# Performance work log

Measured on AMD Instinct MI355X. Metric: run time of the kernel, lower is better.

Reference implementation:

```python
import jax, jax.numpy as jnp
import numpy as np

PAD = 0
SOS = 1
NEG = -1e9


def _lstm_scan(x, Wih, Whh, b, h0, c0, reverse=False):
    # x: [T, B, in]; torch gate order i, f, g, o
    def step(carry, xt):
        h, c = carry
        g = xt @ Wih.T + h @ Whh.T + b
        i, f, gg, o = jnp.split(g, 4, axis=-1)
        c = jax.nn.sigmoid(f) * c + jax.nn.sigmoid(i) * jnp.tanh(gg)
        h = jax.nn.sigmoid(o) * jnp.tanh(c)
        return (h, c), h
    (hT, cT), hs = jax.lax.scan(step, (h0, c0), x, reverse=reverse)
    return hs, hT, cT


def setup_inputs() -> dict:
    B, Ts, Tt = 32, 64, 66
    E, H, V = 512, 512, 16000
    key = jax.random.key(0)
    ks = jax.random.split(key, 16)
    s = 0.05
    n = lambda k, shape: (jax.random.normal(k, shape, dtype=jnp.float32) * s)
    return {
        'src_sentences': jax.random.randint(ks[0], (B, Ts), 4, V),
        'trg_sentences': jax.random.randint(ks[1], (B, Tt), 4, V),
        'src_emb': n(ks[2], (V, E)),
        'trg_emb': n(ks[3], (V, E)),
        'enc0_Wih': n(ks[4], (2, 4 * H, E)),
        'enc0_Whh': n(ks[5], (2, 4 * H, H)),
        'enc0_b': n(ks[6], (2, 4 * H)),
        'enc1_Wih': n(ks[7], (2, 4 * H, 2 * H)),
        'enc1_Whh': n(ks[8], (2, 4 * H, H)),
        'enc1_b': n(ks[9], (2, 4 * H)),
        'dec_Wih': n(ks[10], (8 * H, E)),      # LSTMCell: hidden = 2H -> 4*(2H) gates
        'dec_Whh': n(ks[11], (8 * H, 2 * H)),
        'dec_b': n(ks[12], (8 * H)),
        'out_W1': n(ks[13], (H, 4 * H)),
        'out_W2': n(ks[14], (V - 4, H)),
    }


def reference(src_sentences, trg_sentences, src_emb, trg_emb,
              enc0_Wih, enc0_Whh, enc0_b, enc1_Wih, enc1_Whh, enc1_b,
              dec_Wih, dec_Whh, dec_b, out_W1, out_W2):
    B, Ts = src_sentences.shape
    Tt = trg_sentences.shape[1]
    H = out_W1.shape[0]
    dt = src_emb.dtype
    enc_mask = src_sentences == PAD            # [B, Ts] (all False here)

    # ---- encoder: 2-layer bidirectional LSTM (dropout inactive / eval) ----
    x = jnp.swapaxes(src_emb[src_sentences], 0, 1)   # [Ts, B, E]
    z = jnp.zeros((B, H), dt)
    hf0, hfT, cfT = _lstm_scan(x, enc0_Wih[0], enc0_Whh[0], enc0_b[0], z, z)
    hb0, hbT, cbT = _lstm_scan(x, enc0_Wih[1], enc0_Whh[1], enc0_b[1], z, z, reverse=True)
    x1 = jnp.concatenate([hf0, hb0], axis=-1)        # [Ts, B, 2H]
    hf1, _, _ = _lstm_scan(x1, enc1_Wih[0], enc1_Whh[0], enc1_b[0], z, z)
    hb1, _, _ = _lstm_scan(x1, enc1_Wih[1], enc1_Whh[1], enc1_b[1], z, z, reverse=True)
    enc_out = jnp.swapaxes(jnp.concatenate([hf1, hb1], axis=-1), 0, 1)  # [B, Ts, 2H]
    # module uses encoder_hidden_t[0], [1] -> layer-0 fwd/bwd final states
    hidden = jnp.concatenate([hfT, hbT], axis=-1)    # [B, 2H]
    cell = jnp.concatenate([cfT, cbT], axis=-1)

    # ---- decoder: teacher_force = 1.0 (deterministic) ----
    steps = Tt - 2
    emb_in = jnp.swapaxes(trg_emb[trg_sentences[:, :steps]], 0, 1)  # [steps, B, E]
    tgts = jnp.swapaxes(trg_sentences[:, 1:steps + 1], 0, 1)        # [steps, B]

    def step(carry, inp):
        h, c, loss = carry
        xt, tgt = inp
        g = xt @ dec_Wih.T + h @ dec_Whh.T + dec_b
        i, f, gg, o = jnp.split(g, 4, axis=-1)
        c = jax.nn.sigmoid(f) * c + jax.nn.sigmoid(i) * jnp.tanh(gg)
        h = jax.nn.sigmoid(o) * jnp.tanh(c)
        dmask = tgt == PAD
        h = jnp.where(dmask[:, None], jnp.zeros((), dt), h)  # decoder_hidden_t[mask] = 0
        # dot attention over encoder states
        scores = jnp.einsum('btd,bd->bt', enc_out, h)
        scores = jnp.where(enc_mask, NEG, scores)
        attn = jax.nn.softmax(scores, axis=1)
        ctx = jnp.einsum('bt,btd->bd', attn, enc_out)
        zt = jnp.tanh(jnp.concatenate([h, ctx], axis=-1) @ out_W1.T)
        logits = zt @ out_W2.T                                # [B, V-4]
        logp = jax.nn.log_softmax(logits, axis=1)
        tgt_idx = tgt - 4
        valid = tgt_idx != -4                                 # ignore_index=-4 (PAD)
        safe = jnp.where(valid, tgt_idx, 0)
        nll = -jnp.take_along_axis(logp, safe[:, None], axis=1)[:, 0]
        loss = loss + jnp.sum(jnp.where(valid, nll, jnp.zeros((), dt)))
        pred = jnp.argmax(logits, axis=1) + 4
        return (h, c, loss), pred

    (_, _, loss), preds = jax.lax.scan(step, (hidden, cell, jnp.zeros((), dt)), (emb_in, tgts))
    denom = jnp.sum(trg_sentences[:, 1:-1] != PAD).astype(dt)
    return loss / denom, preds.T  # preds: [B, steps]
```

## Files before the change

kernel.cpp:

```cpp
#include <hip/hip_runtime.h>
#include <hip/hip_bf16.h>
#include <math.h>

#define TSRC 64
#define TTRG 66
#define NVOC 15996
#define NTILE 125

__device__ __forceinline__ float sigm(float x){ return 1.f/(1.f+expf(-x)); }

struct GArgs {
  const float* A;  int lda;
  const float* Bw; int ldb;
  const float* bias;
  float* C; int ldc;
  int N; int K; int nNb; int act;
};

template<int BM,int BN,int BK,int TM,int TN>
__global__ __launch_bounds__(256)
void k_gemm(GArgs a)
{
  const int tid = threadIdx.x;
  const int mb = blockIdx.x / a.nNb;
  const int nb = blockIdx.x % a.nNb;
  const int m0 = mb*BM, n0 = nb*BN;
  const float* A  = a.A + (size_t)m0*a.lda;
  const float* Bw = a.Bw;

  __shared__ float As[BK][BM+1];
  __shared__ float Bs[BK][BN+4];
  const int tx = tid % (BN/TN);
  const int ty = tid / (BN/TN);
  float acc[TM][TN];
  #pragma unroll
  for (int i=0;i<TM;i++)
    #pragma unroll
    for (int j=0;j<TN;j++) acc[i][j]=0.f;

  for (int kt=0; kt<a.K; kt+=BK) {
    #pragma unroll
    for (int i=tid; i<BM*BK; i+=256) {
      int m = i/BK, k = i%BK;
      As[k][m] = A[(size_t)m*a.lda + kt + k];
    }
    #pragma unroll
    for (int i=tid; i<BN*BK; i+=256) {
      int n = i/BK, k = i%BK;
      int gn = n0+n;
      Bs[k][n] = (gn < a.N) ? Bw[(size_t)gn*a.ldb + kt + k] : 0.f;
    }
    __syncthreads();
    #pragma unroll
    for (int k=0;k<BK;k++) {
      float av[TM], bv[TN];
      #pragma unroll
      for (int i=0;i<TM;i++) av[i]=As[k][ty*TM+i];
      #pragma unroll
      for (int j=0;j<TN;j++) bv[j]=Bs[k][tx*TN+j];
      #pragma unroll
      for (int i=0;i<TM;i++)
        #pragma unroll
        for (int j=0;j<TN;j++)
          acc[i][j] = fmaf(av[i], bv[j], acc[i][j]);
    }
    __syncthreads();
  }
  #pragma unroll
  for (int i=0;i<TM;i++) {
    int m = m0 + ty*TM + i;
    #pragma unroll
    for (int j=0;j<TN;j++) {
      int n = n0 + tx*TN + j;
      if (n < a.N) {
        float v = acc[i][j];
        if (a.bias) v += a.bias[n];
        if (a.act)  v = tanhf(v);
        a.C[(size_t)m*a.ldc + n] = v;
      }
    }
  }
}

__global__ __launch_bounds__(256)
void k_logits(const float* __restrict__ A, const float* __restrict__ Bw,
              const int* __restrict__ trg,
              float* __restrict__ Pmax, int* __restrict__ Parg,
              float* __restrict__ Psum, float* __restrict__ Ltgt)
{
  const int tid = threadIdx.x;
  const int mb = blockIdx.x / NTILE;
  const int nb = blockIdx.x % NTILE;
  const int m0 = mb*128, n0 = nb*128;

  __shared__ float As[16][129];
  __shared__ float Bs[16][132];
  const int tx = tid & 15;
  const int ty = tid >> 4;
  float acc[8][8];
  #pragma unroll
  for (int i=0;i<8;i++)
    #pragma unroll
    for (int j=0;j<8;j++) acc[i][j]=0.f;

  for (int kt=0; kt<512; kt+=16) {
    #pragma unroll
    for (int i=tid; i<128*16; i+=256) {
      int m = i>>4, k = i&15;
      As[k][m] = A[(size_t)(m0+m)*512 + kt + k];
    }
    #pragma unroll
    for (int i=tid; i<128*16; i+=256) {
      int n = i>>4, k = i&15;
      int gn = n0+n;
      Bs[k][n] = (gn < NVOC) ? Bw[(size_t)gn*512 + kt + k] : 0.f;
    }
    __syncthreads();
    #pragma unroll
    for (int k=0;k<16;k++) {
      float av[8], bv[8];
      #pragma unroll
      for (int i=0;i<8;i++) av[i]=As[k][ty*8+i];
      #pragma unroll
      for (int j=0;j<8;j++) bv[j]=Bs[k][tx*8+j];
      #pragma unroll
      for (int i=0;i<8;i++)
        #pragma unroll
        for (int j=0;j<8;j++)
          acc[i][j] = fmaf(av[i], bv[j], acc[i][j]);
    }
    __syncthreads();
  }

  #pragma unroll
  for (int i=0;i<8;i++) {
    int r = m0 + ty*8 + i;
    int step = r >> 5, b = r & 31;
    int tgt = trg[b*TTRG + step + 1];
    int ti = tgt - 4;
    float m = -3.4e38f; int am = 0x7fffffff;
    #pragma unroll
    for (int j=0;j<8;j++) {
      int gn = n0 + tx*8 + j;
      if (gn < NVOC) {
        float x = acc[i][j];
        if (x > m || (x == m && gn < am)) { m = x; am = gn; }
      }
    }
    float s = 0.f;
    float lt = 0.f;
    #pragma unroll
    for (int j=0;j<8;j++) {
      int gn = n0 + tx*8 + j;
      if (gn < NVOC) {
        s += expf(acc[i][j] - m);
        if (gn == ti) lt = acc[i][j];
      }
    }
    #pragma unroll
    for (int d=1; d<16; d<<=1) {
      float m2 = __shfl_xor(m, d);
      int   a2 = __shfl_xor(am, d);
      float s2 = __shfl_xor(s, d);
      float l2 = __shfl_xor(lt, d);
      float M = fmaxf(m, m2);
      s = s*expf(m - M) + s2*expf(m2 - M);
      if (m2 > m || (m2 == m && a2 < am)) am = a2;
      m = M;
      lt += l2;
    }
    if (tx == 0) {
      size_t pi = (size_t)r*NTILE + nb;
      Pmax[pi] = m; Parg[pi] = am; Psum[pi] = s;
      if (ti >= n0 && ti < n0 + 128) Ltgt[r] = lt;
    }
  }
}

__global__ __launch_bounds__(128)
void k_combine(const float* __restrict__ Pmax, const int* __restrict__ Parg,
               const float* __restrict__ Psum, const float* __restrict__ Ltgt,
               const int* __restrict__ trg,
               float* __restrict__ nll, float* __restrict__ outp)
{
  int r = blockIdx.x;
  int step = r >> 5, b = r & 31;
  int tid = threadIdx.x;
  __shared__ float sm[128]; __shared__ int sa[128]; __shared__ float ssum[128];
  float m = -3.4e38f; int am = 0x7fffffff; float s = 0.f;
  if (tid < NTILE) {
    size_t pi = (size_t)r*NTILE + tid;
    m = Pmax[pi]; am = Parg[pi]; s = Psum[pi];
  }
  sm[tid]=m; sa[tid]=am; ssum[tid]=s; __syncthreads();
  for (int off=64; off; off>>=1) {
    if (tid < off) {
      float m2 = sm[tid+off]; int a2 = sa[tid+off]; float s2 = ssum[tid+off];
      float m1 = sm[tid];     int a1 = sa[tid];     float s1 = ssum[tid];
      float M = fmaxf(m1, m2);
      ssum[tid] = s1*expf(m1 - M) + s2*expf(m2 - M);
      if (m2 > m1 || (m2 == m1 && a2 < a1)) sa[tid] = a2;
      sm[tid] = M;
    }
    __syncthreads();
  }
  if (tid == 0) {
    int tgt = trg[b*TTRG + step + 1];
    float nl = 0.f;
    if (tgt != 0) nl = -(Ltgt[r] - sm[0] - logf(ssum[0]));
    nll[step*32 + b] = nl;
    outp[1 + b*64 + step] = (float)(sa[0] + 4);
  }
}

__global__ void k_gather(const float* __restrict__ emb, const int* __restrict__ tok,
                         float* __restrict__ outp, int Tfull)
{
  int r = blockIdx.x;
  int t = r >> 5, b = r & 31;
  int token = tok[b*Tfull + t];
  const float4* s = (const float4*)(emb + (size_t)token*512);
  float4* d = (float4*)(outp + (size_t)r*512);
  d[threadIdx.x] = s[threadIdx.x];
}

__global__ __launch_bounds__(256)
void k_rgemm_enc(const float* __restrict__ Whh,
                 const float* __restrict__ hin,
                 float* __restrict__ P)
{
  const int ks  = blockIdx.x >> 5;
  const int rem = blockIdx.x & 31;
  const int dir = rem >> 4;
  const int jt  = rem & 15;
  const int j0  = jt*32;
  const int tid = threadIdx.x;
  const int jcol = tid & 31;
  const int bq   = tid >> 5;
  __shared__ float ws[128][65];
  __shared__ float hs[64][36];
  const float* W = Whh + (size_t)dir*2048*512;
  const float* H = hin + (size_t)dir*32*512;
  float acc[4][4];
  #pragma unroll
  for (int g=0;g<4;g++)
    #pragma unroll
    for (int i=0;i<4;i++) acc[g][i]=0.f;

  for (int kt=ks*128; kt<ks*128+128; kt+=64) {
    for (int idx=tid; idx<128*64; idx+=256) {
      int r = idx >> 6, k = idx & 63;
      int gate = r >> 5, jc = r & 31;
      ws[r][k] = W[(size_t)(gate*512 + j0 + jc)*512 + kt + k];
    }
    for (int idx=tid; idx<32*64; idx+=256) {
      int b = idx >> 6, k = idx & 63;
      hs[k][b] = H[(size_t)b*512 + kt + k];
    }
    __syncthreads();
    #pragma unroll 8
    for (int k=0;k<64;k++) {
      float4 hv = *reinterpret_cast<const float4*>(&hs[k][bq*4]);
      #pragma unroll
      for (int g=0;g<4;g++) {
        float wv = ws[g*32+jcol][k];
        acc[g][0] = fmaf(hv.x, wv, acc[g][0]);
        acc[g][1] = fmaf(hv.y, wv, acc[g][1]);
        acc[g][2] = fmaf(hv.z, wv, acc[g][2]);
        acc[g][3] = fmaf(hv.w, wv, acc[g][3]);
      }
    }
    __syncthreads();
  }
  #pragma unroll
  for (int g=0;g<4;g++)
    #pragma unroll
    for (int i=0;i<4;i++)
      P[((size_t)(ks*2+dir)*32 + bq*4+i)*2048 + g*512 + j0 + jcol] = acc[g][i];
}

__global__ __launch_bounds__(256)
void k_enc_combine(const float* __restrict__ P, const float* __restrict__ xg,
                   float* __restrict__ cst, float* __restrict__ hout,
                   float* __restrict__ xout, int tf, int tb, int mode)
{
  int t = blockIdx.x*256 + threadIdx.x;
  int jh = t & 511, b = (t>>9)&31, dir = t>>14;
  int tt = dir ? tb : tf;
  const float* x = xg + ((size_t)tt*32 + b)*4096 + dir*2048;
  float g4[4];
  #pragma unroll
  for (int g=0; g<4; g++) {
    float s = 0.f;
    #pragma unroll
    for (int ks=0; ks<4; ks++)
      s += P[((size_t)(ks*2+dir)*32 + b)*2048 + g*512 + jh];
    g4[g] = s + x[g*512 + jh];
  }
  size_t ci = ((size_t)dir*32 + b)*512 + jh;
  float cn = sigm(g4[1])*cst[ci] + sigm(g4[0])*tanhf(g4[2]);
  float hn = sigm(g4[3])*tanhf(cn);
  cst[ci] = cn;
  hout[ci] = hn;
  if (mode == 0) xout[((size_t)tt*32 + b)*1024 + dir*512 + jh] = hn;
  else           xout[((size_t)b*64 + tt)*1024 + dir*512 + jh] = hn;
}

__global__ void k_pack(const float* __restrict__ hfin, const float* __restrict__ cfin,
                       float* __restrict__ dh, float* __restrict__ dcc)
{
  int tid = blockIdx.x*256 + threadIdx.x;
  int j = tid & 1023, b = tid >> 10;
  int dir = j >> 9, jj = j & 511;
  size_t si = ((size_t)dir*32 + b)*512 + jj;
  dh[(size_t)b*1024 + j]  = hfin[si];
  dcc[(size_t)b*1024 + j] = cfin[si];
}

__global__ __launch_bounds__(256)
void k_rgemm_dec(const float* __restrict__ Whh,
                 const float* __restrict__ hin,
                 float* __restrict__ P)
{
  const int ks = blockIdx.x >> 5;
  const int jt = blockIdx.x & 31;
  const int j0 = jt*32;
  const int tid = threadIdx.x;
  const int jcol = tid & 31;
  const int bq   = tid >> 5;
  __shared__ float ws[128][65];
  __shared__ float hs[64][36];
  float acc[4][4];
  #pragma unroll
  for (int g=0;g<4;g++)
    #pragma unroll
    for (int i=0;i<4;i++) acc[g][i]=0.f;

  for (int kt=ks*128; kt<ks*128+128; kt+=64) {
    for (int idx=tid; idx<128*64; idx+=256) {
      int r = idx >> 6, k = idx & 63;
      int gate = r >> 5, jc = r & 31;
      ws[r][k] = Whh[(size_t)(gate*1024 + j0 + jc)*1024 + kt + k];
    }
    for (int idx=tid; idx<32*64; idx+=256) {
      int b = idx >> 6, k = idx & 63;
      hs[k][b] = hin[(size_t)b*1024 + kt + k];
    }
    __syncthreads();
    #pragma unroll 8
    for (int k=0;k<64;k++) {
      float4 hv = *reinterpret_cast<const float4*>(&hs[k][bq*4]);
      #pragma unroll
      for (int g=0;g<4;g++) {
        float wv = ws[g*32+jcol][k];
        acc[g][0] = fmaf(hv.x, wv, acc[g][0]);
        acc[g][1] = fmaf(hv.y, wv, acc[g][1]);
        acc[g][2] = fmaf(hv.z, wv, acc[g][2]);
        acc[g][3] = fmaf(hv.w, wv, acc[g][3]);
      }
    }
    __syncthreads();
  }
  #pragma unroll
  for (int g=0;g<4;g++)
    #pragma unroll
    for (int i=0;i<4;i++)
      P[((size_t)ks*32 + bq*4+i)*4096 + g*1024 + j0 + jcol] = acc[g][i];
}

__global__ __launch_bounds__(256)
void k_dec_combine(const float* __restrict__ P, const float* __restrict__ xg_t,
                   float* __restrict__ cst, float* __restrict__ hall_t,
                   const int* __restrict__ trg, int step)
{
  int t = blockIdx.x*256 + threadIdx.x;
  int jh = t & 1023, b = t >> 10;
  int tgt = trg[b*TTRG + step + 1];
  bool dm = (tgt == 0);
  const float* x = xg_t + (size_t)b*4096;
  float g4[4];
  #pragma unroll
  for (int g=0; g<4; g++) {
    float s = 0.f;
    #pragma unroll
    for (int ks=0; ks<8; ks++)
      s += P[((size_t)ks*32 + b)*4096 + g*1024 + jh];
    g4[g] = s + x[g*1024 + jh];
  }
  size_t ci = (size_t)b*1024 + jh;
  float cn = sigm(g4[1])*cst[ci] + sigm(g4[0])*tanhf(g4[2]);
  float hn = sigm(g4[3])*tanhf(cn);
  cst[ci] = cn;
  hall_t[ci] = dm ? 0.f : hn;
}

__global__ __launch_bounds__(256)
void k_attn(const float* __restrict__ Hall,
            const float* __restrict__ encout,
            const int* __restrict__ src,
            float* __restrict__ hctx)
{
  int bid = blockIdx.x;
  int t = bid >> 5, b = bid & 31;
  int tid = threadIdx.x;
  __shared__ float sh[1024];
  __shared__ float ssc[64];
  const float* h = Hall + ((size_t)t*32 + b)*1024;
  size_t row = (size_t)t*32 + b;
  #pragma unroll
  for (int r=0;r<4;r++) {
    int jh = tid + 256*r;
    float v = h[jh];
    sh[jh] = v;
    hctx[row*2048 + jh] = v;
  }
  __syncthreads();
  {
    int tq = tid >> 2, part = tid & 3;
    const float* eo = encout + ((size_t)b*64 + tq)*1024 + part*256;
    const float* hh = sh + part*256;
    float s = 0.f;
    for (int k=0;k<256;k++) s = fmaf(hh[k], eo[k], s);
    s += __shfl_xor(s, 1);
    s += __shfl_xor(s, 2);
    if (part == 0) ssc[tq] = (src[b*TSRC + tq] == 0) ? -1e9f : s;
  }
  __syncthreads();
  if (tid < 64) {
    float v = ssc[tid];
    float m = v;
    for (int d=1; d<64; d<<=1) m = fmaxf(m, __shfl_xor(m, d));
    float e = expf(v - m);
    float su = e;
    for (int d=1; d<64; d<<=1) su += __shfl_xor(su, d);
    ssc[tid] = e / su;
  }
  __syncthreads();
  #pragma unroll
  for (int r=0;r<4;r++) {
    int k = tid + 256*r;
    float a = 0.f;
    const float* eb = encout + (size_t)b*65536 + k;
    for (int tt=0;tt<64;tt++) a = fmaf(ssc[tt], eb[tt*1024], a);
    hctx[row*2048 + 1024 + k] = a;
  }
}

__global__ __launch_bounds__(256)
void k_final(const float* __restrict__ nll, const int* __restrict__ trg,
             float* __restrict__ outp)
{
  int tid = threadIdx.x;
  __shared__ float ss[256]; __shared__ int sc[256];
  float s = 0.f; int cnt = 0;
  for (int i=tid; i<2048; i+=256) {
    s += nll[i];
    int b = i >> 6, t = (i & 63) + 1;
    cnt += (trg[b*TTRG + t] != 0);
  }
  ss[tid]=s; sc[tid]=cnt; __syncthreads();
  for (int off=128; off; off>>=1) {
    if (tid<off) { ss[tid]+=ss[tid+off]; sc[tid]+=sc[tid+off]; }
    __syncthreads();
  }
  if (tid==0) outp[0] = ss[0] / (float)sc[0];
}

static void launch_big(hipStream_t st, const float* A, int lda,
                       const float* Bw, int ldb, const float* bias,
                       float* C, int ldc, int M, int N, int K, int act)
{
  GArgs a;
  a.A=A; a.lda=lda;
  a.Bw=Bw; a.ldb=ldb;
  a.bias=bias;
  a.C=C; a.ldc=ldc;
  a.N=N; a.K=K; a.nNb=(N+127)/128; a.act=act;
  dim3 g((M/128)*a.nNb, 1, 1);
  k_gemm<128,128,16,8,8><<<g, dim3(256), 0, st>>>(a);
}

static void launch_med(hipStream_t st, const float* A, int lda,
                       const float* Bw, int ldb, const float* bias,
                       float* C, int ldc, int M, int N, int K, int act)
{
  GArgs a;
  a.A=A; a.lda=lda;
  a.Bw=Bw; a.ldb=ldb;
  a.bias=bias;
  a.C=C; a.ldc=ldc;
  a.N=N; a.K=K; a.nNb=(N+63)/64; a.act=act;
  dim3 g((M/64)*a.nNb, 1, 1);
  k_gemm<64,64,16,4,4><<<g, dim3(256), 0, st>>>(a);
}

extern "C" void kernel_launch(void* const* d_in, const int* in_sizes, int n_in,
                              void* d_out, int out_size, void* d_ws, size_t ws_size,
                              hipStream_t stream)
{
  (void)in_sizes; (void)n_in; (void)out_size; (void)ws_size;
  const int*   src   = (const int*)  d_in[0];
  const int*   trg   = (const int*)  d_in[1];
  const float* semb  = (const float*)d_in[2];
  const float* temb  = (const float*)d_in[3];
  const float* e0Wih = (const float*)d_in[4];
  const float* e0Whh = (const float*)d_in[5];
  const float* e0b   = (const float*)d_in[6];
  const float* e1Wih = (const float*)d_in[7];
  const float* e1Whh = (const float*)d_in[8];
  const float* e1b   = (const float*)d_in[9];
  const float* dWih  = (const float*)d_in[10];
  const float* dWhh  = (const float*)d_in[11];
  const float* db    = (const float*)d_in[12];
  const float* W1    = (const float*)d_in[13];
  const float* W2    = (const float*)d_in[14];
  float* out = (float*)d_out;

  float* ws = (float*)d_ws;
  size_t o = 0;
  float* x_in   = ws + o; o += (size_t)2048*512;
  float* xg     = ws + o; o += (size_t)2048*4096;
  float* x1     = ws + o; o += (size_t)2048*1024;
  float* encout = ws + o; o += (size_t)2048*1024;
  float* hA     = ws + o; o += 2*32*512;
  float* hB     = ws + o; o += 2*32*512;
  float* cbuf   = ws + o; o += 2*32*512;
  float* dh0    = ws + o; o += 32*1024;
  float* dc     = ws + o; o += 32*1024;
  float* nll    = ws + o; o += 2048;
  float* P      = ws + o; o += (size_t)8*32*4096;
  float* Hall   = x1;
  float* hctx   = xg;
  float* zt     = x_in;
  float* Pmax   = xg + (size_t)4*1024*1024;
  int*   Parg   = (int*)(Pmax + (size_t)2048*NTILE);
  float* Psum   = Pmax + (size_t)2*2048*NTILE;
  float* Ltgt   = Pmax + (size_t)3*2048*NTILE;

  hipMemsetAsync(hA,   0, 2*32*512*sizeof(float), stream);
  hipMemsetAsync(cbuf, 0, 2*32*512*sizeof(float), stream);
  k_gather<<<dim3(2048), dim3(128), 0, stream>>>(semb, src, x_in, TSRC);
  launch_big(stream, x_in, 512, e0Wih, 512, e0b, xg, 4096, 2048, 4096, 512, 0);
  for (int s=0; s<64; s++) {
    float* hin  = (s&1) ? hB : hA;
    float* hout = (s&1) ? hA : hB;
    k_rgemm_enc<<<dim3(128), dim3(256), 0, stream>>>(e0Whh, hin, P);
    k_enc_combine<<<dim3(128), dim3(256), 0, stream>>>(P, xg, cbuf, hout, x1, s, 63-s, 0);
  }
  k_pack<<<dim3(128), dim3(256), 0, stream>>>(hA, cbuf, dh0, dc);

  hipMemsetAsync(hA,   0, 2*32*512*sizeof(float), stream);
  hipMemsetAsync(cbuf, 0, 2*32*512*sizeof(float), stream);
  launch_big(stream, x1, 1024, e1Wih, 1024, e1b, xg, 4096, 2048, 4096, 1024, 0);
  for (int s=0; s<64; s++) {
    float* hin  = (s&1) ? hB : hA;
    float* hout = (s&1) ? hA : hB;
    k_rgemm_enc<<<dim3(128), dim3(256), 0, stream>>>(e1Whh, hin, P);
    k_enc_combine<<<dim3(128), dim3(256), 0, stream>>>(P, xg, cbuf, hout, encout, s, 63-s, 1);
  }

  k_gather<<<dim3(2048), dim3(128), 0, stream>>>(temb, trg, x_in, TTRG);
  launch_big(stream, x_in, 512, dWih, 512, db, xg, 4096, 2048, 4096, 512, 0);
  for (int st=0; st<64; st++) {
    const float* hin = (st == 0) ? dh0 : (Hall + (size_t)(st-1)*32*1024);
    k_rgemm_dec<<<dim3(256), dim3(256), 0, stream>>>(dWhh, hin, P);
    k_dec_combine<<<dim3(128), dim3(256), 0, stream>>>(P, xg + (size_t)st*32*4096,
                 dc, Hall + (size_t)st*32*1024, trg, st);
  }

  k_attn<<<dim3(2048), dim3(256), 0, stream>>>(Hall, encout, src, hctx);
  launch_med(stream, hctx, 2048, W1, 2048, nullptr, zt, 512, 2048, 512, 2048, 1);
  k_logits<<<dim3(16*NTILE), dim3(256), 0, stream>>>(zt, W2, trg, Pmax, Parg, Psum, Ltgt);
  k_combine<<<dim3(2048), dim3(128), 0, stream>>>(Pmax, Parg, Psum, Ltgt, trg, nll, out);
  k_final<<<dim3(1), dim3(256), 0, stream>>>(nll, trg, out);
}
```

Before: 4.647 ms.

## Fuse recurrent LSTM steps into persistent kernels with grid barriers

Replaces the per-timestep launch pairs (recurrent GEMM plus gate combine) for both encoder layers and the decoder with single persistent kernels that loop over all 64 steps and use an atomic-counter grid barrier between phases. This removes about 384 kernel launches and their launch gaps. In exchange it relies on all 128/256 blocks being co-resident for the spin barrier to avoid deadlock. The weights are still reloaded from global memory every step, and each step now pays two barrier round trips.

```diff
diff --git a/kernel.cpp b/kernel.cpp
--- a/kernel.cpp
+++ b/kernel.cpp
@@ -8,6 +8,20 @@
 #define NTILE 125
 
 __device__ __forceinline__ float sigm(float x){ return 1.f/(1.f+expf(-x)); }
+
+__device__ __forceinline__ void grid_barrier(unsigned* cnt, unsigned nblk, unsigned& mygen)
+{
+  __syncthreads();
+  if (threadIdx.x == 0) {
+    __threadfence();
+    atomicAdd(cnt, 1u);
+    unsigned target = nblk * (mygen + 1u);
+    while (atomicAdd(cnt, 0u) < target) __builtin_amdgcn_s_sleep(2);
+    __threadfence();
+  }
+  __syncthreads();
+  mygen += 1u;
+}
 
 struct GArgs {
   const float* A;  int lda;
@@ -225,12 +239,17 @@
 }
 
 __global__ __launch_bounds__(256)
-void k_rgemm_enc(const float* __restrict__ Whh,
-                 const float* __restrict__ hin,
-                 float* __restrict__ P)
-{
-  const int ks  = blockIdx.x >> 5;
-  const int rem = blockIdx.x & 31;
+void k_enc_layer(const float* __restrict__ Whh,
+                 const float* __restrict__ xg,
+                 float* __restrict__ hA, float* __restrict__ hB,
+                 float* __restrict__ cst,
+                 float* __restrict__ P,
+                 float* __restrict__ xout, int mode,
+                 unsigned* __restrict__ cnt)
+{
+  const int bid = blockIdx.x;
+  const int ks  = bid >> 5;
+  const int rem = bid & 31;
   const int dir = rem >> 4;
   const int jt  = rem & 15;
   const int j0  = jt*32;
@@ -240,70 +259,77 @@
   __shared__ float ws[128][65];
   __shared__ float hs[64][36];
   const float* W = Whh + (size_t)dir*2048*512;
-  const float* H = hin + (size_t)dir*32*512;
-  float acc[4][4];
-  #pragma unroll
-  for (int g=0;g<4;g++)
-    #pragma unroll
-    for (int i=0;i<4;i++) acc[g][i]=0.f;
-
-  for (int kt=ks*128; kt<ks*128+128; kt+=64) {
-    for (int idx=tid; idx<128*64; idx+=256) {
-      int r = idx >> 6, k = idx & 63;
-      int gate = r >> 5, jc = r & 31;
-      ws[r][k] = W[(size_t)(gate*512 + j0 + jc)*512 + kt + k];
-    }
-    for (int idx=tid; idx<32*64; idx+=256) {
-      int b = idx >> 6, k = idx & 63;
-      hs[k][b] = H[(size_t)b*512 + kt + k];
-    }
-    __syncthreads();
-    #pragma unroll 8
-    for (int k=0;k<64;k++) {
-      float4 hv = *reinterpret_cast<const float4*>(&hs[k][bq*4]);
-      #pragma unroll
-      for (int g=0;g<4;g++) {
-        float wv = ws[g*32+jcol][k];
-        acc[g][0] = fmaf(hv.x, wv, acc[g][0]);
-        acc[g][1] = fmaf(hv.y, wv, acc[g][1]);
-        acc[g][2] = fmaf(hv.z, wv, acc[g][2]);
-        acc[g][3] = fmaf(hv.w, wv, acc[g][3]);
-      }
-    }
-    __syncthreads();
-  }
-  #pragma unroll
-  for (int g=0;g<4;g++)
-    #pragma unroll
-    for (int i=0;i<4;i++)
-      P[((size_t)(ks*2+dir)*32 + bq*4+i)*2048 + g*512 + j0 + jcol] = acc[g][i];
-}
-
-__global__ __launch_bounds__(256)
-void k_enc_combine(const float* __restrict__ P, const float* __restrict__ xg,
-                   float* __restrict__ cst, float* __restrict__ hout,
-                   float* __restrict__ xout, int tf, int tb, int mode)
-{
-  int t = blockIdx.x*256 + threadIdx.x;
-  int jh = t & 511, b = (t>>9)&31, dir = t>>14;
-  int tt = dir ? tb : tf;
-  const float* x = xg + ((size_t)tt*32 + b)*4096 + dir*2048;
-  float g4[4];
-  #pragma unroll
-  for (int g=0; g<4; g++) {
-    float s = 0.f;
-    #pragma unroll
-    for (int ks=0; ks<4; ks++)
-      s += P[((size_t)(ks*2+dir)*32 + b)*2048 + g*512 + jh];
-    g4[g] = s + x[g*512 + jh];
-  }
-  size_t ci = ((size_t)dir*32 + b)*512 + jh;
-  float cn = sigm(g4[1])*cst[ci] + sigm(g4[0])*tanhf(g4[2]);
-  float hn = sigm(g4[3])*tanhf(cn);
-  cst[ci] = cn;
-  hout[ci] = hn;
-  if (mode == 0) xout[((size_t)tt*32 + b)*1024 + dir*512 + jh] = hn;
-  else           xout[((size_t)b*64 + tt)*1024 + dir*512 + jh] = hn;
+  unsigned mygen = 0;
+
+  for (int s = 0; s < 64; ++s) {
+    const float* hin = (s&1) ? hB : hA;
+    float* hout      = (s&1) ? hA : hB;
+    const float* H = hin + (size_t)dir*32*512;
+    float acc[4][4];
+    #pragma unroll
+    for (int g=0;g<4;g++)
+      #pragma unroll
+      for (int i=0;i<4;i++) acc[g][i]=0.f;
+
+    for (int kh=0; kh<2; ++kh) {
+      int kt = ks*128 + kh*64;
+      for (int idx=tid; idx<128*64; idx+=256) {
+        int r = idx >> 6, k = idx & 63;
+        int gate = r >> 5, jc = r & 31;
+        ws[r][k] = W[(size_t)(gate*512 + j0 + jc)*512 + kt + k];
+      }
+      for (int idx=tid; idx<32*64; idx+=256) {
+        int b = idx >> 6, k = idx & 63;
+        hs[k][b] = H[(size_t)b*512 + kt + k];
+      }
+      __syncthreads();
+      #pragma unroll 8
+      for (int k=0;k<64;k++) {
+        float4 hv = *reinterpret_cast<const float4*>(&hs[k][bq*4]);
+        #pragma unroll
+        for (int g=0;g<4;g++) {
+          float wv = ws[g*32+jcol][k];
+          acc[g][0] = fmaf(hv.x, wv, acc[g][0]);
+          acc[g][1] = fmaf(hv.y, wv, acc[g][1]);
+          acc[g][2] = fmaf(hv.z, wv, acc[g][2]);
+          acc[g][3] = fmaf(hv.w, wv, acc[g][3]);
+        }
+      }
+      __syncthreads();
+    }
+    #pragma unroll
+    for (int g=0;g<4;g++)
+      #pragma unroll
+      for (int i=0;i<4;i++)
+        P[((size_t)(ks*2+dir)*32 + bq*4+i)*2048 + g*512 + j0 + jcol] = acc[g][i];
+
+    grid_barrier(cnt, 128u, mygen);
+
+    {
+      int t = bid*256 + tid;
+      int jh = t & 511, b = (t>>9)&31, d2 = t>>14;
+      int tt = d2 ? (63 - s) : s;
+      const float* x = xg + ((size_t)tt*32 + b)*4096 + d2*2048;
+      float g4[4];
+      #pragma unroll
+      for (int g=0; g<4; g++) {
+        float sum = 0.f;
+        #pragma unroll
+        for (int kk=0; kk<4; kk++)
+          sum += P[((size_t)(kk*2+d2)*32 + b)*2048 + g*512 + jh];
+        g4[g] = sum + x[g*512 + jh];
+      }
+      size_t ci = ((size_t)d2*32 + b)*512 + jh;
+      float cn = sigm(g4[1])*cst[ci] + sigm(g4[0])*tanhf(g4[2]);
+      float hn = sigm(g4[3])*tanhf(cn);
+      cst[ci] = cn;
+      hout[ci] = hn;
+      if (mode == 0) xout[((size_t)tt*32 + b)*1024 + d2*512 + jh] = hn;
+      else           xout[((size_t)b*64 + tt)*1024 + d2*512 + jh] = hn;
+    }
+
+    grid_barrier(cnt, 128u, mygen);
+  }
 }
 
 __global__ void k_pack(const float* __restrict__ hfin, const float* __restrict__ cfin,
@@ -318,9 +344,14 @@
 }
 
 __global__ __launch_bounds__(256)
-void k_rgemm_dec(const float* __restrict__ Whh,
-                 const float* __restrict__ hin,
-                 float* __restrict__ P)
+void k_dec_layer(const float* __restrict__ Whh,
+                 const float* __restrict__ xg,
+                 const float* __restrict__ dh0,
+                 float* __restrict__ cst,
+                 float* __restrict__ Hall,
+                 const int* __restrict__ trg,
+                 float* __restrict__ P,
+                 unsigned* __restrict__ cnt)
 {
   const int ks = blockIdx.x >> 5;
   const int jt = blockIdx.x & 31;
@@ -330,68 +361,74 @@
   const int bq   = tid >> 5;
   __shared__ float ws[128][65];
   __shared__ float hs[64][36];
-  float acc[4][4];
-  #pragma unroll
-  for (int g=0;g<4;g++)
-    #pragma unroll
-    for (int i=0;i<4;i++) acc[g][i]=0.f;
-
-  for (int kt=ks*128; kt<ks*128+128; kt+=64) {
-    for (int idx=tid; idx<128*64; idx+=256) {
-      int r = idx >> 6, k = idx & 63;
-      int gate = r >> 5, jc = r & 31;
-      ws[r][k] = Whh[(size_t)(gate*1024 + j0 + jc)*1024 + kt + k];
-    }
-    for (int idx=tid; idx<32*64; idx+=256) {
-      int b = idx >> 6, k = idx & 63;
-      hs[k][b] = hin[(size_t)b*1024 + kt + k];
-    }
-    __syncthreads();
-    #pragma unroll 8
-    for (int k=0;k<64;k++) {
-      float4 hv = *reinterpret_cast<const float4*>(&hs[k][bq*4]);
-      #pragma unroll
-      for (int g=0;g<4;g++) {
-        float wv = ws[g*32+jcol][k];
-        acc[g][0] = fmaf(hv.x, wv, acc[g][0]);
-        acc[g][1] = fmaf(hv.y, wv, acc[g][1]);
-        acc[g][2] = fmaf(hv.z, wv, acc[g][2]);
-        acc[g][3] = fmaf(hv.w, wv, acc[g][3]);
-      }
-    }
-    __syncthreads();
-  }
-  #pragma unroll
-  for (int g=0;g<4;g++)
-    #pragma unroll
-    for (int i=0;i<4;i++)
-      P[((size_t)ks*32 + bq*4+i)*4096 + g*1024 + j0 + jcol] = acc[g][i];
-}
-
-__global__ __launch_bounds__(256)
-void k_dec_combine(const float* __restrict__ P, const float* __restrict__ xg_t,
-                   float* __restrict__ cst, float* __restrict__ hall_t,
-                   const int* __restrict__ trg, int step)
-{
-  int t = blockIdx.x*256 + threadIdx.x;
-  int jh = t & 1023, b = t >> 10;
-  int tgt = trg[b*TTRG + step + 1];
-  bool dm = (tgt == 0);
-  const float* x = xg_t + (size_t)b*4096;
-  float g4[4];
-  #pragma unroll
-  for (int g=0; g<4; g++) {
-    float s = 0.f;
-    #pragma unroll
-    for (int ks=0; ks<8; ks++)
-      s += P[((size_t)ks*32 + b)*4096 + g*1024 + jh];
-    g4[g] = s + x[g*1024 + jh];
-  }
-  size_t ci = (size_t)b*1024 + jh;
-  float cn = sigm(g4[1])*cst[ci] + sigm(g4[0])*tanhf(g4[2]);
-  float hn = sigm(g4[3])*tanhf(cn);
-  cst[ci] = cn;
-  hall_t[ci] = dm ? 0.f : hn;
+  unsigned mygen = 0;
+
+  for (int st = 0; st < 64; ++st) {
+    const float* hin = (st == 0) ? dh0 : (Hall + (size_t)(st-1)*32*1024);
+    float acc[4][4];
+    #pragma unroll
+    for (int g=0;g<4;g++)
+      #pragma unroll
+      for (int i=0;i<4;i++) acc[g][i]=0.f;
+
+    for (int kh=0; kh<2; ++kh) {
+      int kt = ks*128 + kh*64;
+      for (int idx=tid; idx<128*64; idx+=256) {
+        int r = idx >> 6, k = idx & 63;
+        int gate = r >> 5, jc = r & 31;
+        ws[r][k] = Whh[(size_t)(gate*1024 + j0 + jc)*1024 + kt + k];
+      }
+      for (int idx=tid; idx<32*64; idx+=256) {
+        int b = idx >> 6, k = idx & 63;
+        hs[k][b] = hin[(size_t)b*1024 + kt + k];
+      }
+      __syncthreads();
+      #pragma unroll 8
+      for (int k=0;k<64;k++) {
+        float4 hv = *reinterpret_cast<const float4*>(&hs[k][bq*4]);
+        #pragma unroll
+        for (int g=0;g<4;g++) {
+          float wv = ws[g*32+jcol][k];
+          acc[g][0] = fmaf(hv.x, wv, acc[g][0]);
+          acc[g][1] = fmaf(hv.y, wv, acc[g][1]);
+          acc[g][2] = fmaf(hv.z, wv, acc[g][2]);
+          acc[g][3] = fmaf(hv.w, wv, acc[g][3]);
+        }
+      }
+      __syncthreads();
+    }
+    #pragma unroll
+    for (int g=0;g<4;g++)
+      #pragma unroll
+      for (int i=0;i<4;i++)
+        P[((size_t)ks*32 + bq*4+i)*4096 + g*1024 + j0 + jcol] = acc[g][i];
+
+    grid_barrier(cnt, 256u, mygen);
+
+    if (tid < 128) {
+      int t = blockIdx.x*128 + tid;
+      int jh = t & 1023, b = t >> 10;
+      int tgt = trg[b*TTRG + st + 1];
+      bool dm = (tgt == 0);
+      const float* x = xg + (size_t)st*32*4096 + (size_t)b*4096;
+      float g4[4];
+      #pragma unroll
+      for (int g=0; g<4; g++) {
+        float sum = 0.f;
+        #pragma unroll
+        for (int kk=0; kk<8; kk++)
+          sum += P[((size_t)kk*32 + b)*4096 + g*1024 + jh];
+        g4[g] = sum + x[g*1024 + jh];
+      }
+      size_t ci = (size_t)b*1024 + jh;
+      float cn = sigm(g4[1])*cst[ci] + sigm(g4[0])*tanhf(g4[2]);
+      float hn = sigm(g4[3])*tanhf(cn);
+      cst[ci] = cn;
+      Hall[(size_t)st*32*1024 + ci] = dm ? 0.f : hn;
+    }
+
+    grid_barrier(cnt, 256u, mygen);
+  }
 }
 
 __global__ __launch_bounds__(256)
@@ -529,6 +566,7 @@
   float* dc     = ws + o; o += 32*1024;
   float* nll    = ws + o; o += 2048;
   float* P      = ws + o; o += (size_t)8*32*4096;
+  unsigned* cnt = (unsigned*)(ws + o); o += 64;
   float* Hall   = x1;
   float* hctx   = xg;
   float* zt     = x_in;
@@ -537,36 +575,26 @@
   float* Psum   = Pmax + (size_t)2*2048*NTILE;
   float* Ltgt   = Pmax + (size_t)3*2048*NTILE;
 
+  hipMemsetAsync(cnt, 0, 64*sizeof(float), stream);
+
   hipMemsetAsync(hA,   0, 2*32*512*sizeof(float), stream);
   hipMemsetAsync(cbuf, 0, 2*32*512*sizeof(float), stream);
   k_gather<<<dim3(2048), dim3(128), 0, stream>>>(semb, src, x_in, TSRC);
   launch_big(stream, x_in, 512, e0Wih, 512, e0b, xg, 4096, 2048, 4096, 512, 0);
-  for (int s=0; s<64; s++) {
-    float* hin  = (s&1) ? hB : hA;
-    float* hout = (s&1) ? hA : hB;
-    k_rgemm_enc<<<dim3(128), dim3(256), 0, stream>>>(e0Whh, hin, P);
-    k_enc_combine<<<dim3(128), dim3(256), 0, stream>>>(P, xg, cbuf, hout, x1, s, 63-s, 0);
-  }
+  k_enc_layer<<<dim3(128), dim3(256), 0, stream>>>(e0Whh, xg, hA, hB, cbuf, P,
+                                                   x1, 0, cnt);
   k_pack<<<dim3(128), dim3(256), 0, stream>>>(hA, cbuf, dh0, dc);
 
   hipMemsetAsync(hA,   0, 2*32*512*sizeof(float), stream);
   hipMemsetAsync(cbuf, 0, 2*32*512*sizeof(float), stream);
   launch_big(stream, x1, 1024, e1Wih, 1024, e1b, xg, 4096, 2048, 4096, 1024, 0);
-  for (int s=0; s<64; s++) {
-    float* hin  = (s&1) ? hB : hA;
-    float* hout = (s&1) ? hA : hB;
-    k_rgemm_enc<<<dim3(128), dim3(256), 0, stream>>>(e1Whh, hin, P);
-    k_enc_combine<<<dim3(128), dim3(256), 0, stream>>>(P, xg, cbuf, hout, encout, s, 63-s, 1);
-  }
+  k_enc_layer<<<dim3(128), dim3(256), 0, stream>>>(e1Whh, xg, hA, hB, cbuf, P,
+                                                   encout, 1, cnt + 16);
 
   k_gather<<<dim3(2048), dim3(128), 0, stream>>>(temb, trg, x_in, TTRG);
   launch_big(stream, x_in, 512, dWih, 512, db, xg, 4096, 2048, 4096, 512, 0);
-  for (int st=0; st<64; st++) {
-    const float* hin = (st == 0) ? dh0 : (Hall + (size_t)(st-1)*32*1024);
-    k_rgemm_dec<<<dim3(256), dim3(256), 0, stream>>>(dWhh, hin, P);
-    k_dec_combine<<<dim3(128), dim3(256), 0, stream>>>(P, xg + (size_t)st*32*4096,
-                 dc, Hall + (size_t)st*32*1024, trg, st);
-  }
+  k_dec_layer<<<dim3(256), dim3(256), 0, stream>>>(dWhh, xg, dh0, dc, Hall, trg,
+                                                   P, cnt + 32);
 
   k_attn<<<dim3(2048), dim3(256), 0, stream>>>(Hall, encout, src, hctx);
   launch_med(stream, hctx, 2048, W1, 2048, nullptr, zt, 512, 2048, 512, 2048, 1);
```

Result: slower. 9.716 ms (+109.1%).
